# Optimization experiments

Measured on AMD Instinct MI355X. Metric: run time of the kernel, lower is better.

Reference implementation:

```python
import jax, jax.numpy as jnp
import numpy as np

N_NODES = 100000
N_EDGES = 1600000
IN_DIM = 128
HID_DIM = 64


def setup_inputs() -> dict:
    key = jax.random.key(0)
    k = jax.random.split(key, 8)
    x = jax.random.normal(k[0], (N_NODES, IN_DIM), dtype=jnp.float32)
    edge_index = jax.random.randint(k[1], (2, N_EDGES), 0, N_NODES, dtype=jnp.int64)
    perm = jax.random.randint(k[2], (N_NODES,), 0, N_NODES, dtype=jnp.int64)
    # learned parameters
    W_gcn = jax.random.normal(k[3], (IN_DIM, HID_DIM), dtype=jnp.float32) / np.sqrt(IN_DIM)
    b_gcn = jnp.zeros((HID_DIM,), dtype=jnp.float32)
    prelu_a = jnp.full((HID_DIM,), 0.25, dtype=jnp.float32)  # nn.PReLU default init
    W_disc = jax.random.normal(k[4], (HID_DIM, HID_DIM), dtype=jnp.float32) / np.sqrt(HID_DIM)
    return {"x": x, "W_gcn": W_gcn, "b_gcn": b_gcn, "prelu_a": prelu_a,
            "W_disc": W_disc, "edge_index": edge_index, "perm": perm}


def _gcn_conv(x, W, b, src, dst, n_nodes):
    """PyG GCNConv: linear transform, add self-loops, symmetric deg^-1/2 norm, scatter-add."""
    h = x @ W  # [N, hid]
    loop = jnp.arange(n_nodes, dtype=src.dtype)
    src = jnp.concatenate([src, loop])
    dst = jnp.concatenate([dst, loop])
    deg = jax.ops.segment_sum(jnp.ones_like(dst, h.dtype), dst, num_segments=n_nodes)
    dinv = jax.lax.rsqrt(deg)  # deg >= 1 thanks to self-loops
    norm = dinv[src] * dinv[dst]  # [E+N]
    msg = h[src] * norm[:, None]  # [E+N, hid] -- dominant gather
    out = jax.ops.segment_sum(msg, dst, num_segments=n_nodes)
    return out + b


def _prelu(x, a):
    return jnp.where(x > 0, x, x * a)


def reference(x, W_gcn, b_gcn, prelu_a, W_disc, edge_index, perm):
    n_nodes = x.shape[0]
    src, dst = edge_index[0], edge_index[1]
    # positive view
    pos = _prelu(_gcn_conv(x, W_gcn, b_gcn, src, dst, n_nodes), prelu_a)
    # negative (corrupted) view: permuted node features, same graph
    neg = _prelu(_gcn_conv(x[perm], W_gcn, b_gcn, src, dst, n_nodes), prelu_a)
    # summary vector
    summary = jax.nn.sigmoid(pos.mean(axis=0))  # [hid]
    s = W_disc @ summary  # [hid]
    pos_logit = pos @ s  # [N]
    neg_logit = neg @ s  # [N]
    # BCEWithLogitsLoss(pos, ones) + BCEWithLogitsLoss(neg, zeros)
    l1 = jnp.mean(jax.nn.softplus(-pos_logit))
    l2 = jnp.mean(jax.nn.softplus(neg_logit))
    return l1 + l2
```

## Files before the change

### kernel.cpp

```cpp
#include <hip/hip_runtime.h>

#define HID 64
#define INDIM 128
#define NBUCK 256
#define EBUF_PER 10240
#define PAD_PER 14336
#define CHUNK 4096
#define RMASK 0x1FFFFu

typedef unsigned short ushort_t;
typedef unsigned int uint_t;
typedef float floatx2 __attribute__((ext_vector_type(2)));

__device__ __forceinline__ float softplusf(float x) {
    return fmaxf(x, 0.f) + log1pf(expf(-fabsf(x)));
}
__device__ __forceinline__ float dec_norm(uint_t x) {
    union { uint_t i; float f; } c; c.i = (x >> 17) << 16; return c.f;
}

__global__ __launch_bounds__(256) void k_fused(const float* __restrict__ x,
                                               const float* __restrict__ W,
                                               const int* __restrict__ src,
                                               const int* __restrict__ dst,
                                               uint_t* __restrict__ Hq,
                                               int* __restrict__ bcur,
                                               int2* __restrict__ ebuf,
                                               int N, int E, int nbA) {
    __shared__ char lds[66560];
    int tid = threadIdx.x;

    if ((int)blockIdx.x < nbA) {
        int2* stage  = (int2*)lds;
        int* lcnt    = (int*)(lds + 32768);
        int* binSt   = (int*)(lds + 33792);
        int* lofs    = (int*)(lds + 34816);
        int* gofs    = (int*)(lds + 35840);
        int* scn     = (int*)(lds + 36864);
        int base = blockIdx.x * CHUNK;

        lcnt[tid] = 0;
        __syncthreads();

        int sv[16], dv[16];
#pragma unroll
        for (int i = 0; i < 16; i++) {
            int e = base + i * 256 + tid;
            if (e < E) { sv[i] = src[e]; dv[i] = dst[e]; }
            else dv[i] = -1;
        }
#pragma unroll
        for (int i = 0; i < 16; i++)
            if (dv[i] >= 0) atomicAdd(&lcnt[dv[i] >> 9], 1);
        __syncthreads();

        scn[tid] = lcnt[tid];
        __syncthreads();
        for (int off = 1; off < NBUCK; off <<= 1) {
            int v = (tid >= off) ? scn[tid - off] : 0;
            __syncthreads();
            scn[tid] += v;
            __syncthreads();
        }
        binSt[tid] = scn[tid] - lcnt[tid];
        lofs[tid] = binSt[tid];
        __syncthreads();

#pragma unroll
        for (int i = 0; i < 16; i++) {
            if (dv[i] >= 0) {
                int b = dv[i] >> 9;
                int p = atomicAdd(&lofs[b], 1);
                stage[p] = make_int2(sv[i], dv[i]);
            }
        }
        __syncthreads();

        if (lcnt[tid] > 0)
            gofs[tid] = tid * EBUF_PER + atomicAdd(&bcur[tid], lcnt[tid]);
        __syncthreads();

        int total = (base + CHUNK <= E) ? CHUNK : (E > base ? E - base : 0);
        for (int idx = tid; idx < total; idx += 256) {
            int2 v = stage[idx];
            int b = v.y >> 9;
            ebuf[gofs[b] + (idx - binSt[b])] = v;
        }
    } else {
        float* Xs = (float*)lds;
        float* Ws = (float*)(lds + 33792);
        int row0 = ((int)blockIdx.x - nbA) * 64;

        const float4* W4 = (const float4*)W;
        float4* Ws4 = (float4*)Ws;
#pragma unroll
        for (int i = 0; i < 8; i++) Ws4[tid + 256 * i] = W4[tid + 256 * i];

#pragma unroll
        for (int i = 0; i < 8; i++) {
            int j = tid + 256 * i;
            int r = j >> 5, c4 = j & 31;
            int row = row0 + r;
            float4 v = make_float4(0.f, 0.f, 0.f, 0.f);
            if (row < N) v = *(const float4*)(x + (size_t)row * INDIM + c4 * 4);
            *(float4*)(&Xs[r * 132 + c4 * 4]) = v;
        }
        __syncthreads();

        int tx = tid & 15;
        int ty = tid >> 4;
        float acc[4][4] = {};
        const float* xa = &Xs[(ty * 4) * 132];
#pragma unroll 4
        for (int k4 = 0; k4 < 32; k4++) {
            float4 x0 = *(const float4*)(&xa[k4 * 4]);
            float4 x1 = *(const float4*)(&xa[132 + k4 * 4]);
            float4 x2 = *(const float4*)(&xa[264 + k4 * 4]);
            float4 x3 = *(const float4*)(&xa[396 + k4 * 4]);
#pragma unroll
            for (int kk = 0; kk < 4; kk++) {
                float4 bv = *(const float4*)(&Ws[(k4 * 4 + kk) * 64 + tx * 4]);
                float a0 = ((const float*)&x0)[kk];
                float a1 = ((const float*)&x1)[kk];
                float a2 = ((const float*)&x2)[kk];
                float a3 = ((const float*)&x3)[kk];
                acc[0][0] = fmaf(a0, bv.x, acc[0][0]);
                acc[0][1] = fmaf(a0, bv.y, acc[0][1]);
                acc[0][2] = fmaf(a0, bv.z, acc[0][2]);
                acc[0][3] = fmaf(a0, bv.w, acc[0][3]);
                acc[1][0] = fmaf(a1, bv.x, acc[1][0]);
                acc[1][1] = fmaf(a1, bv.y, acc[1][1]);
                acc[1][2] = fmaf(a1, bv.z, acc[1][2]);
                acc[1][3] = fmaf(a1, bv.w, acc[1][3]);
                acc[2][0] = fmaf(a2, bv.x, acc[2][0]);
                acc[2][1] = fmaf(a2, bv.y, acc[2][1]);
                acc[2][2] = fmaf(a2, bv.z, acc[2][2]);
                acc[2][3] = fmaf(a2, bv.w, acc[2][3]);
                acc[3][0] = fmaf(a3, bv.x, acc[3][0]);
                acc[3][1] = fmaf(a3, bv.y, acc[3][1]);
                acc[3][2] = fmaf(a3, bv.z, acc[3][2]);
                acc[3][3] = fmaf(a3, bv.w, acc[3][3]);
            }
        }
#pragma unroll
        for (int i = 0; i < 4; i++) {
            int row = row0 + ty * 4 + i;
            if (row < N) {
                uint_t u = 0;
                u = __builtin_amdgcn_cvt_pk_fp8_f32(acc[i][0], acc[i][1], u, false);
                u = __builtin_amdgcn_cvt_pk_fp8_f32(acc[i][2], acc[i][3], u, true);
                Hq[(size_t)row * 16 + tx] = u;
            }
        }
    }
}

__global__ __launch_bounds__(256) void k_hc(const uint_t* __restrict__ Hq,
                                            const int* __restrict__ perm,
                                            uint_t* __restrict__ HC, int N) {
    int g = blockIdx.x * 256 + threadIdx.x;
    if (g >= N * 16) return;
    int n = g >> 4, sub = g & 15;
    HC[(size_t)n * 32 + sub] = Hq[(size_t)n * 16 + sub];
    HC[(size_t)n * 32 + 16 + sub] = Hq[(size_t)perm[n] * 16 + sub];
}

__global__ __launch_bounds__(256) void k_binB1(const int2* __restrict__ ebuf,
                                               const int* __restrict__ bcur,
                                               int* __restrict__ rowptr,
                                               float* __restrict__ dinvg,
                                               int N) {
    __shared__ int sc[256];
    __shared__ int ldeg[512];
    int tid = threadIdx.x;
    int b = blockIdx.x;

    ldeg[tid] = 0;
    ldeg[tid + 256] = 0;
    __syncthreads();

    int start = b * EBUF_PER;
    int cb = bcur[b];
    for (int i = start + tid; i < start + cb; i += 256)
        atomicAdd(&ldeg[ebuf[i].y & 511], 1);
    __syncthreads();

    int d0 = ldeg[2 * tid], d1 = ldeg[2 * tid + 1];
    int p0 = (d0 + 7) & ~7, p1 = (d1 + 7) & ~7;
    int s2 = p0 + p1;
    sc[tid] = s2;
    __syncthreads();
    for (int off = 1; off < 256; off <<= 1) {
        int v = (tid >= off) ? sc[tid - off] : 0;
        __syncthreads();
        sc[tid] += v;
        __syncthreads();
    }
    int ex = sc[tid] - s2;
    int n0 = (b << 9) + 2 * tid, n1 = n0 + 1;
    int prow0 = b * PAD_PER + ex;
    int prow1 = prow0 + p0;
    if (n0 < N) { rowptr[n0] = prow0 | ((p0 >> 3) << 23); dinvg[n0] = rsqrtf((float)(d0 + 1)); }
    if (n1 < N) { rowptr[n1] = prow1 | ((p1 >> 3) << 23); dinvg[n1] = rsqrtf((float)(d1 + 1)); }
}

__global__ __launch_bounds__(256) void k_binB2(const int2* __restrict__ ebuf,
                                               const int* __restrict__ bcur,
                                               const int* __restrict__ rowptr,
                                               const float* __restrict__ dinvg,
                                               uint_t* __restrict__ csrS, int N) {
    __shared__ int lcur[512];
    __shared__ float ldinv[512];
    int tid = threadIdx.x;
    int b = blockIdx.x;
    int nodeBase = b << 9;
    for (int i = tid; i < 512; i += 256) {
        int n = nodeBase + i;
        lcur[i] = (n < N) ? (rowptr[n] & 0x7FFFFF) : 0;
        ldinv[i] = (n < N) ? dinvg[n] : 0.f;
    }
    __syncthreads();

    int start = b * EBUF_PER;
    int cb = bcur[b];
    for (int i = start + tid; i < start + cb; i += 256) {
        int2 v = ebuf[i];
        int s = v.x, dl = v.y & 511;
        int j = atomicAdd(&lcur[dl], 1);
        float nm = dinvg[s] * ldinv[dl];
        union { float f; uint_t u; } cu; cu.f = nm;
        uint_t nb = (cu.u >> 16) & 0x7FFFu;
        csrS[j] = (uint_t)s | (nb << 17);
    }
    __syncthreads();

    for (int i = tid; i < 512; i += 256) {
        int n = nodeBase + i;
        if (n < N) {
            uint_t r = (uint_t)rowptr[n];
            int e = (int)(r & 0x7FFFFF) + 8 * (int)(r >> 23);
            for (int j = lcur[i]; j < e; j++) csrS[j] = 0u;
        }
    }
}

__global__ __launch_bounds__(256) void k_gather(const uint_t* __restrict__ HC,
                                                const int* __restrict__ rowptr,
                                                const uint_t* __restrict__ csrS,
                                                const float* __restrict__ dinv,
                                                const float* __restrict__ b,
                                                const float* __restrict__ a,
                                                uint_t* __restrict__ posq,
                                                uint_t* __restrict__ negq,
                                                float* __restrict__ sumvec, int N) {
    int tid = threadIdx.x;
    int lane = tid & 63;
    int slot = lane >> 4;
    int sub = lane & 15;
    int isneg = slot & 1;
    int pair = slot >> 1;
    int hoff = isneg * 16 + sub;
    int wid = (blockIdx.x * 256 + tid) >> 6;
    int nw = gridDim.x * 4;
    float4 b4 = ((const float4*)b)[sub];
    float4 a4 = ((const float4*)a)[sub];
    float s0 = 0.f, s1 = 0.f, s2 = 0.f, s3 = 0.f;

    for (int n = wid; n < N; n += nw) {
        float dv = dinv[n];
        float w2 = dv * dv;
        uint_t r = (uint_t)rowptr[n];
        int beg = (int)(r & 0x7FFFFF);
        int iters = (int)(r >> 23);
        float a0 = 0.f, a1 = 0.f, a2 = 0.f, a3 = 0.f;

        int base0 = beg + pair;
        uint_t cA0 = csrS[base0];
        uint_t cA1 = csrS[base0 + 2];
        uint_t cA2 = csrS[base0 + 4];
        uint_t cA3 = csrS[base0 + 6];
        uint_t cB0 = csrS[base0 + 8];
        uint_t cB1 = csrS[base0 + 10];
        uint_t cB2 = csrS[base0 + 12];
        uint_t cB3 = csrS[base0 + 14];
        uint_t uc0 = HC[(size_t)(cA0 & RMASK) * 32 + hoff];
        uint_t uc1 = HC[(size_t)(cA1 & RMASK) * 32 + hoff];
        uint_t uc2 = HC[(size_t)(cA2 & RMASK) * 32 + hoff];
        uint_t uc3 = HC[(size_t)(cA3 & RMASK) * 32 + hoff];

        for (int it = 0; it < iters; it++) {
            int gbase = base0 + (it + 2) * 8;
            uint_t cC0 = csrS[gbase];
            uint_t cC1 = csrS[gbase + 2];
            uint_t cC2 = csrS[gbase + 4];
            uint_t cC3 = csrS[gbase + 6];
            uint_t un0 = HC[(size_t)(cB0 & RMASK) * 32 + hoff];
            uint_t un1 = HC[(size_t)(cB1 & RMASK) * 32 + hoff];
            uint_t un2 = HC[(size_t)(cB2 & RMASK) * 32 + hoff];
            uint_t un3 = HC[(size_t)(cB3 & RMASK) * 32 + hoff];
            float mA0 = dec_norm(cA0);
            float mA1 = dec_norm(cA1);
            float mA2 = dec_norm(cA2);
            float mA3 = dec_norm(cA3);
            floatx2 lo, hi;
            lo = __builtin_amdgcn_cvt_pk_f32_fp8(uc0, false);
            hi = __builtin_amdgcn_cvt_pk_f32_fp8(uc0, true);
            a0 = fmaf(lo.x, mA0, a0); a1 = fmaf(lo.y, mA0, a1);
            a2 = fmaf(hi.x, mA0, a2); a3 = fmaf(hi.y, mA0, a3);
            lo = __builtin_amdgcn_cvt_pk_f32_fp8(uc1, false);
            hi = __builtin_amdgcn_cvt_pk_f32_fp8(uc1, true);
            a0 = fmaf(lo.x, mA1, a0); a1 = fmaf(lo.y, mA1, a1);
            a2 = fmaf(hi.x, mA1, a2); a3 = fmaf(hi.y, mA1, a3);
            lo = __builtin_amdgcn_cvt_pk_f32_fp8(uc2, false);
            hi = __builtin_amdgcn_cvt_pk_f32_fp8(uc2, true);
            a0 = fmaf(lo.x, mA2, a0); a1 = fmaf(lo.y, mA2, a1);
            a2 = fmaf(hi.x, mA2, a2); a3 = fmaf(hi.y, mA2, a3);
            lo = __builtin_amdgcn_cvt_pk_f32_fp8(uc3, false);
            hi = __builtin_amdgcn_cvt_pk_f32_fp8(uc3, true);
            a0 = fmaf(lo.x, mA3, a0); a1 = fmaf(lo.y, mA3, a1);
            a2 = fmaf(hi.x, mA3, a2); a3 = fmaf(hi.y, mA3, a3);
            cA0 = cB0; cA1 = cB1; cA2 = cB2; cA3 = cB3;
            cB0 = cC0; cB1 = cC1; cB2 = cC2; cB3 = cC3;
            uc0 = un0; uc1 = un1; uc2 = un2; uc3 = un3;
        }
        a0 += __shfl_xor(a0, 32);
        a1 += __shfl_xor(a1, 32);
        a2 += __shfl_xor(a2, 32);
        a3 += __shfl_xor(a3, 32);
        uint_t us = HC[(size_t)n * 32 + hoff];
        floatx2 slo = __builtin_amdgcn_cvt_pk_f32_fp8(us, false);
        floatx2 shi = __builtin_amdgcn_cvt_pk_f32_fp8(us, true);
        float v0 = fmaf(slo.x, w2, a0) + b4.x;
        float v1 = fmaf(slo.y, w2, a1) + b4.y;
        float v2 = fmaf(shi.x, w2, a2) + b4.z;
        float v3 = fmaf(shi.y, w2, a3) + b4.w;
        v0 = v0 > 0.f ? v0 : v0 * a4.x;
        v1 = v1 > 0.f ? v1 : v1 * a4.y;
        v2 = v2 > 0.f ? v2 : v2 * a4.z;
        v3 = v3 > 0.f ? v3 : v3 * a4.w;
        if (lane < 32) {
            uint_t pk = 0;
            pk = __builtin_amdgcn_cvt_pk_fp8_f32(v0, v1, pk, false);
            pk = __builtin_amdgcn_cvt_pk_fp8_f32(v2, v3, pk, true);
            uint_t* outp = isneg ? negq : posq;
            outp[(size_t)n * 16 + sub] = pk;
            if (!isneg) { s0 += v0; s1 += v1; s2 += v2; s3 += v3; }
        }
    }

    __shared__ float red[4][64];
    int w = tid >> 6;
    if (slot == 0) {
        red[w][sub * 4 + 0] = s0;
        red[w][sub * 4 + 1] = s1;
        red[w][sub * 4 + 2] = s2;
        red[w][sub * 4 + 3] = s3;
    }
    __syncthreads();
    if (tid < 64) {
        float s = red[0][tid] + red[1][tid] + red[2][tid] + red[3][tid];
        atomicAdd(&sumvec[tid], s);
    }
}

__global__ __launch_bounds__(256) void k_loss(const uint_t* __restrict__ posq,
                                              const uint_t* __restrict__ negq,
                                              float* __restrict__ smallb,
                                              const float* __restrict__ Wd,
                                              float* __restrict__ out, int N) {
    __shared__ float summ[64];
    __shared__ float svecS[64];
    __shared__ float redL[4][4];
    int tid = threadIdx.x;
    float* sumvec = smallb;
    float* lossAcc = smallb + 128;
    int* done = (int*)(smallb + 129);

    if (tid < 64) summ[tid] = 1.f / (1.f + expf(-sumvec[tid] / (float)N));
    __syncthreads();
    if (tid < 64) {
        float s = 0.f;
#pragma unroll
        for (int j = 0; j < 64; j++) s += Wd[tid * 64 + j] * summ[j];
        svecS[tid] = s;
    }
    __syncthreads();

    int lane = tid & 63;
    int slot = lane >> 4;
    int sub = lane & 15;
    int isneg = slot & 1;
    int pair = slot >> 1;
    int w = tid >> 6;
    float4 sv = ((const float4*)svecS)[sub];
    const uint_t* Pb = isneg ? negq : posq;
    float l = 0.f;
    int wid = (blockIdx.x * 256 + tid) >> 6;
    int nw = gridDim.x * 4;
    for (int g = wid; 2 * g < N; g += nw) {
        int row = 2 * g + pair;
        bool valid = row < N;
        uint_t u = valid ? Pb[(size_t)row * 16 + sub] : 0u;
        floatx2 lo = __builtin_amdgcn_cvt_pk_f32_fp8(u, false);
        floatx2 hi = __builtin_amdgcn_cvt_pk_f32_fp8(u, true);
        float p = lo.x * sv.x + lo.y * sv.y + hi.x * sv.z + hi.y * sv.w;
        p += __shfl_xor(p, 1);
        p += __shfl_xor(p, 2);
        p += __shfl_xor(p, 4);
        p += __shfl_xor(p, 8);
        if (sub == 0 && valid) l += isneg ? softplusf(p) : softplusf(-p);
    }
    if (sub == 0) redL[w][slot] = l;
    __syncthreads();
    if (tid == 0) {
        float t = 0.f;
#pragma unroll
        for (int i = 0; i < 4; i++)
#pragma unroll
            for (int j = 0; j < 4; j++) t += redL[i][j];
        atomicAdd(&lossAcc[0], t);
        __threadfence();
        int old = atomicAdd(done, 1);
        if (old == (int)gridDim.x - 1) {
            float tot = atomicAdd(&lossAcc[0], 0.f);
            out[0] = tot / (float)N;
        }
    }
}

extern "C" void kernel_launch(void* const* d_in, const int* in_sizes, int n_in,
                              void* d_out, int out_size, void* d_ws, size_t ws_size,
                              hipStream_t stream) {
    const float* x      = (const float*)d_in[0];
    const float* W_gcn  = (const float*)d_in[1];
    const float* b_gcn  = (const float*)d_in[2];
    const float* prelu_a= (const float*)d_in[3];
    const float* W_disc = (const float*)d_in[4];
    const int*   eidx   = (const int*)d_in[5];
    const int*   perm   = (const int*)d_in[6];

    int N = in_sizes[0] / INDIM;
    int E = in_sizes[5] / 2;
    const int* src = eidx;
    const int* dst = eidx + E;

    char* base = (char*)d_ws;
    size_t off = 0;
    auto alloc = [&](size_t bytes) { size_t o = off; off = (off + bytes + 255) & ~(size_t)255; return o; };
    uint_t*   Hq    = (uint_t*)  (base + alloc((size_t)N * HID));
    uint_t*   HC    = (uint_t*)  (base + alloc(((size_t)0x20000 * 32) * 4));
    uint_t*   posq  = (uint_t*)  (base + alloc((size_t)N * HID));
    uint_t*   negq  = (uint_t*)  (base + alloc((size_t)N * HID));
    uint_t*   csrS  = (uint_t*)  (base + alloc(((size_t)NBUCK * PAD_PER + 64) * 4));
    int2*     ebuf  = (int2*)   (base + alloc((size_t)NBUCK * EBUF_PER * 8));
    int*      rowptr= (int*)    (base + alloc(((size_t)N + 1) * 4));
    float*    dinv  = (float*)  (base + alloc((size_t)N * 4));
    size_t zOff = alloc(NBUCK * 4 + 132 * 4);
    int*      bcur  = (int*)(base + zOff);
    float*    smallb= (float*)(base + zOff + NBUCK * 4);
    float* sumvec = smallb;

    int nbA = (E + CHUNK - 1) / CHUNK;
    int nbG = (N + 63) / 64;
    int nbB = (N + 511) / 512;
    int nbH = (N * 16 + 255) / 256;

    hipMemsetAsync(bcur, 0, NBUCK * 4 + 132 * 4, stream);
    k_fused<<<nbA + nbG, 256, 0, stream>>>(x, W_gcn, src, dst, Hq, bcur, ebuf, N, E, nbA);
    k_hc<<<nbH, 256, 0, stream>>>(Hq, perm, HC, N);
    k_binB1<<<nbB, 256, 0, stream>>>(ebuf, bcur, rowptr, dinv, N);
    k_binB2<<<nbB, 256, 0, stream>>>(ebuf, bcur, rowptr, dinv, csrS, N);
    k_gather<<<2048, 256, 0, stream>>>(HC, rowptr, csrS, dinv,
                                       b_gcn, prelu_a, posq, negq, sumvec, N);
    k_loss<<<512, 256, 0, stream>>>(posq, negq, smallb, W_disc, (float*)d_out, N);
}
```

Measured before the change: 200.7 us.

## Compute x@W projection with bf16 MFMA instead of scalar FP32 FMAs

Replaces the per-thread 4x4 FP32 FMA tile in the projection blocks of the fused kernel with bf16 MFMA 16x16x32 instructions. X and a transposed W are converted to bf16 in LDS, and results are staged through LDS before fp8 packing. The LDS footprint shrinks, which may raise occupancy for the edge-binning blocks that share the kernel. Precision drops from fp32 to bf16 inputs, though the output is already fp8-quantized.

```diff
diff --git a/kernel.cpp b/kernel.cpp
--- a/kernel.cpp
+++ b/kernel.cpp
@@ -11,9 +11,17 @@
 typedef unsigned short ushort_t;
 typedef unsigned int uint_t;
 typedef float floatx2 __attribute__((ext_vector_type(2)));
+typedef short bf16x8 __attribute__((ext_vector_type(8)));
+typedef float f32x4 __attribute__((ext_vector_type(4)));
 
 __device__ __forceinline__ float softplusf(float x) {
     return fmaxf(x, 0.f) + log1pf(expf(-fabsf(x)));
+}
+__device__ __forceinline__ ushort_t f2bf(float f) {
+    union { float f; uint_t i; } c; c.f = f;
+    uint_t u = c.i;
+    u += 0x7FFFu + ((u >> 16) & 1u);
+    return (ushort_t)(u >> 16);
 }
 __device__ __forceinline__ float dec_norm(uint_t x) {
     union { uint_t i; float f; } c; c.i = (x >> 17) << 16; return c.f;
@@ -27,7 +35,7 @@
                                                int* __restrict__ bcur,
                                                int2* __restrict__ ebuf,
                                                int N, int E, int nbA) {
-    __shared__ char lds[66560];
+    __shared__ char lds[37888];
     int tid = threadIdx.x;
 
     if ((int)blockIdx.x < nbA) {
@@ -87,69 +95,81 @@
             ebuf[gofs[b] + (idx - binSt[b])] = v;
         }
     } else {
-        float* Xs = (float*)lds;
-        float* Ws = (float*)(lds + 33792);
+        ushort_t* Wt = (ushort_t*)lds;
+        ushort_t* Xs = (ushort_t*)(lds + 17408);
+        float*    Cs = (float*)(lds + 17408);
         int row0 = ((int)blockIdx.x - nbA) * 64;
 
         const float4* W4 = (const float4*)W;
-        float4* Ws4 = (float4*)Ws;
-#pragma unroll
-        for (int i = 0; i < 8; i++) Ws4[tid + 256 * i] = W4[tid + 256 * i];
-
 #pragma unroll
         for (int i = 0; i < 8; i++) {
-            int j = tid + 256 * i;
-            int r = j >> 5, c4 = j & 31;
+            int idx4 = tid + 256 * i;
+            float4 v = W4[idx4];
+            int gidx = idx4 * 4;
+            int k = gidx >> 6, c = gidx & 63;
+            Wt[(c + 0) * 136 + k] = f2bf(v.x);
+            Wt[(c + 1) * 136 + k] = f2bf(v.y);
+            Wt[(c + 2) * 136 + k] = f2bf(v.z);
+            Wt[(c + 3) * 136 + k] = f2bf(v.w);
+        }
+#pragma unroll
+        for (int i = 0; i < 8; i++) {
+            int idx4 = tid + 256 * i;
+            int gidx = idx4 * 4;
+            int r = gidx >> 7, k = gidx & 127;
             int row = row0 + r;
             float4 v = make_float4(0.f, 0.f, 0.f, 0.f);
-            if (row < N) v = *(const float4*)(x + (size_t)row * INDIM + c4 * 4);
-            *(float4*)(&Xs[r * 132 + c4 * 4]) = v;
-        }
-        __syncthreads();
-
-        int tx = tid & 15;
-        int ty = tid >> 4;
-        float acc[4][4] = {};
-        const float* xa = &Xs[(ty * 4) * 132];
-#pragma unroll 4
-        for (int k4 = 0; k4 < 32; k4++) {
-            float4 x0 = *(const float4*)(&xa[k4 * 4]);
-            float4 x1 = *(const float4*)(&xa[132 + k4 * 4]);
-            float4 x2 = *(const float4*)(&xa[264 + k4 * 4]);
-            float4 x3 = *(const float4*)(&xa[396 + k4 * 4]);
-#pragma unroll
-            for (int kk = 0; kk < 4; kk++) {
-                float4 bv = *(const float4*)(&Ws[(k4 * 4 + kk) * 64 + tx * 4]);
-                float a0 = ((const float*)&x0)[kk];
-                float a1 = ((const float*)&x1)[kk];
-                float a2 = ((const float*)&x2)[kk];
-                float a3 = ((const float*)&x3)[kk];
-                acc[0][0] = fmaf(a0, bv.x, acc[0][0]);
-                acc[0][1] = fmaf(a0, bv.y, acc[0][1]);
-                acc[0][2] = fmaf(a0, bv.z, acc[0][2]);
-                acc[0][3] = fmaf(a0, bv.w, acc[0][3]);
-                acc[1][0] = fmaf(a1, bv.x, acc[1][0]);
-                acc[1][1] = fmaf(a1, bv.y, acc[1][1]);
-                acc[1][2] = fmaf(a1, bv.z, acc[1][2]);
-                acc[1][3] = fmaf(a1, bv.w, acc[1][3]);
-                acc[2][0] = fmaf(a2, bv.x, acc[2][0]);
-                acc[2][1] = fmaf(a2, bv.y, acc[2][1]);
-                acc[2][2] = fmaf(a2, bv.z, acc[2][2]);
-                acc[2][3] = fmaf(a2, bv.w, acc[2][3]);
-                acc[3][0] = fmaf(a3, bv.x, acc[3][0]);
-                acc[3][1] = fmaf(a3, bv.y, acc[3][1]);
-                acc[3][2] = fmaf(a3, bv.z, acc[3][2]);
-                acc[3][3] = fmaf(a3, bv.w, acc[3][3]);
-            }
-        }
+            if (row < N) v = *(const float4*)(x + (size_t)row * INDIM + k);
+            ushort4 o;
+            o.x = f2bf(v.x); o.y = f2bf(v.y); o.z = f2bf(v.z); o.w = f2bf(v.w);
+            *(ushort4*)(&Xs[r * 136 + k]) = o;
+        }
+        __syncthreads();
+
+        int wv = tid >> 6, l = tid & 63;
+        int lr = l & 15, kb = l >> 4;
+        int arow = wv * 16 + lr;
+        f32x4 acc0 = {0.f, 0.f, 0.f, 0.f};
+        f32x4 acc1 = {0.f, 0.f, 0.f, 0.f};
+        f32x4 acc2 = {0.f, 0.f, 0.f, 0.f};
+        f32x4 acc3 = {0.f, 0.f, 0.f, 0.f};
+#pragma unroll
+        for (int ks = 0; ks < 4; ks++) {
+            int k0 = ks * 32 + kb * 8;
+            bf16x8 af = *(const bf16x8*)(&Xs[arow * 136 + k0]);
+            bf16x8 b0 = *(const bf16x8*)(&Wt[(0 * 16 + lr) * 136 + k0]);
+            bf16x8 b1 = *(const bf16x8*)(&Wt[(1 * 16 + lr) * 136 + k0]);
+            bf16x8 b2 = *(const bf16x8*)(&Wt[(2 * 16 + lr) * 136 + k0]);
+            bf16x8 b3 = *(const bf16x8*)(&Wt[(3 * 16 + lr) * 136 + k0]);
+            acc0 = __builtin_amdgcn_mfma_f32_16x16x32_bf16(af, b0, acc0, 0, 0, 0);
+            acc1 = __builtin_amdgcn_mfma_f32_16x16x32_bf16(af, b1, acc1, 0, 0, 0);
+            acc2 = __builtin_amdgcn_mfma_f32_16x16x32_bf16(af, b2, acc2, 0, 0, 0);
+            acc3 = __builtin_amdgcn_mfma_f32_16x16x32_bf16(af, b3, acc3, 0, 0, 0);
+        }
+        __syncthreads();
+#pragma unroll
+        for (int j = 0; j < 4; j++) {
+            int crow = wv * 16 + (l >> 4) * 4 + j;
+            Cs[crow * 64 + 0 * 16 + lr] = acc0[j];
+            Cs[crow * 64 + 1 * 16 + lr] = acc1[j];
+            Cs[crow * 64 + 2 * 16 + lr] = acc2[j];
+            Cs[crow * 64 + 3 * 16 + lr] = acc3[j];
+        }
+        __syncthreads();
 #pragma unroll
         for (int i = 0; i < 4; i++) {
-            int row = row0 + ty * 4 + i;
+            int idx = tid + 256 * i;
+            int r = idx >> 4, c4 = idx & 15;
+            int row = row0 + r;
             if (row < N) {
+                float v0 = Cs[r * 64 + c4 * 4 + 0];
+                float v1 = Cs[r * 64 + c4 * 4 + 1];
+                float v2 = Cs[r * 64 + c4 * 4 + 2];
+                float v3 = Cs[r * 64 + c4 * 4 + 3];
                 uint_t u = 0;
-                u = __builtin_amdgcn_cvt_pk_fp8_f32(acc[i][0], acc[i][1], u, false);
-                u = __builtin_amdgcn_cvt_pk_fp8_f32(acc[i][2], acc[i][3], u, true);
-                Hq[(size_t)row * 16 + tx] = u;
+                u = __builtin_amdgcn_cvt_pk_fp8_f32(v0, v1, u, false);
+                u = __builtin_amdgcn_cvt_pk_fp8_f32(v2, v3, u, true);
+                Hq[(size_t)row * 16 + c4] = u;
             }
         }
     }
```

New measurement: 183.2 us. 8.7% less time.
